# Kernel optimization log

Hardware: AMD Instinct MI355X
Metric: run time of the kernel (lower is better)

The kernel has to match this reference:

```python
import jax, jax.numpy as jnp
import numpy as np

B, N, F, H, OUT = 64, 512, 128, 256, 6


def setup_inputs() -> dict:
    key = jax.random.key(0)
    ks = jax.random.split(key, 20)
    s = 0.02
    inp = {
        "x": jax.random.normal(ks[0], (B * N, F), dtype=jnp.float32),
        "edge_index": jax.random.randint(ks[1], (2, 16), 0, B * N),
        "edge_weight": jax.random.uniform(ks[2], (16,), dtype=jnp.float32),
        "batch": jnp.repeat(jnp.arange(B, dtype=jnp.int64), N),
        "sigma": jax.random.uniform(ks[3], (1,), dtype=jnp.float32),
        "Wg": s * jax.random.normal(ks[4], (F, F)), "bg": jnp.zeros((F,)),
        "Wrel0": s * jax.random.normal(ks[5], (F, H)), "Wroot0": s * jax.random.normal(ks[6], (F, H)), "brel0": jnp.zeros((H,)),
        "Wrel1": s * jax.random.normal(ks[7], (H, H)), "Wroot1": s * jax.random.normal(ks[8], (H, H)), "brel1": jnp.zeros((H,)),
        "Wrel2": s * jax.random.normal(ks[9], (H, H)), "Wroot2": s * jax.random.normal(ks[10], (H, H)), "brel2": jnp.zeros((H,)),
        "W1": s * jax.random.normal(ks[11], (H, H)), "b1": jnp.zeros((H,)),
        "Wout": s * jax.random.normal(ks[12], (H, OUT)), "bout": jnp.zeros((OUT,)),
    }
    return inp


def _forward(x, sigma, Wg, bg, Wrel0, Wroot0, brel0, Wrel1, Wroot1, brel1,
             Wrel2, Wroot2, brel2, W1, b1, Wout, bout):
    # gdmLinear
    h = x @ Wg + bg                      # [B*N, F]
    hw = h.reshape(B, N, -1)             # to_dense_batch (equal-size windows)
    # pairwise squared distances per window -> Gaussian kernel
    sq = jnp.sum(hw * hw, axis=-1)       # [B, N]
    dist = jnp.maximum(sq[:, :, None] + sq[:, None, :]
                       - 2.0 * jnp.einsum('bnf,bmf->bnm', hw, hw), 0.0)
    A = jnp.exp(-dist / (2.0 * sigma[0] ** 2))   # [B, N, N], all > 0
    A = A * (1.0 - jnp.eye(N, dtype=A.dtype))    # nonzero extraction drops self-loops

    def conv(h, Wrel, Wroot, brel):
        # GraphConv: out_i = W_rel @ sum_j A[j,i] * h_j + b_rel + W_root @ h_i
        agg = jnp.einsum('bji,bjf->bif', A, h)
        return agg @ Wrel + brel + h @ Wroot

    h = hw
    h = jax.nn.relu(conv(h, Wrel0, Wroot0, brel0))
    h = jax.nn.relu(conv(h, Wrel1, Wroot1, brel1))
    h = conv(h, Wrel2, Wroot2, brel2)
    g = jnp.mean(h, axis=1)              # global_mean_pool (equal-size graphs)
    g = jax.nn.relu(g @ W1 + b1)
    return g @ Wout + bout               # [B, OUT]


def reference(x, edge_index, edge_weight, batch, sigma, Wg, bg,
              Wrel0, Wroot0, brel0, Wrel1, Wroot1, brel1,
              Wrel2, Wroot2, brel2, W1, b1, Wout, bout):
    # edge_index / edge_weight / batch inputs are recomputed internally by GdmGNN
    return _forward(x, sigma, Wg, bg, Wrel0, Wroot0, brel0, Wrel1, Wroot1, brel1,
                    Wrel2, Wroot2, brel2, W1, b1, Wout, bout)
```

## Files before the change

### kernel.cpp

```cpp
#include <hip/hip_runtime.h>
#include <math.h>

#define Bsz 64
#define Nn 512
#define Ff 128
#define Hh 256
#define OUTD 6
#define MTOT (Bsz * Nn)

typedef __bf16 bf16x8 __attribute__((ext_vector_type(8)));
typedef float f32x4 __attribute__((ext_vector_type(4)));
typedef int int4v __attribute__((ext_vector_type(4)));
typedef unsigned short ushort4v __attribute__((ext_vector_type(4)));

__device__ __forceinline__ unsigned short f2bf(float f) {
    unsigned u = __float_as_uint(f);
    u += 0x7FFFu + ((u >> 16) & 1u);
    return (unsigned short)(u >> 16);
}
__device__ __forceinline__ float bf2f(unsigned short s) {
    return __uint_as_float(((unsigned)s) << 16);
}

#define SWZ(r) (((r) ^ ((r) >> 2)) & 3)

__device__ __forceinline__ void async_ld16(const unsigned short* g, unsigned short* l) {
    __builtin_amdgcn_global_load_lds(
        (const __attribute__((address_space(1))) void*)g,
        (__attribute__((address_space(3))) void*)l,
        16, 0, 0);
}

#define LDH 40
#define TSZ (128 * 32)
#define ATS (256 * 32)
#define AGP 136
#define AGP1 264

__global__ __launch_bounds__(512) void fused_l0(
    const unsigned short* __restrict__ h0T,
    const unsigned short* __restrict__ Arows,
    const unsigned short* __restrict__ h0b,
    const unsigned short* __restrict__ WrelT0,
    const unsigned short* __restrict__ WrootT0,
    const float* __restrict__ brel0,
    unsigned short* __restrict__ h1b,
    unsigned short* __restrict__ h1T)
{
    int id = blockIdx.x;
    int b = id & 63;
    int nt = id >> 6;
    int n0g = nt * 128;
    long nodeBase = (long)b * Nn + n0g;

    const unsigned short* HT = h0T + (long)b * Ff * Nn;
    const unsigned short* AR = Arows + (long)b * Nn * Nn;

    __shared__ unsigned short SA[2 * ATS];
    __shared__ unsigned short SB[2 * TSZ];
    __shared__ unsigned short aggL[128 * AGP];

    int tid = threadIdx.x;
    int lane = tid & 63;
    int wave = tid >> 6;
    int quad = lane >> 4, l16 = lane & 15;
    int sr = lane >> 2, sc = lane & 3;

    {
        int wm = (wave >> 1) * 32, wn = (wave & 1) * 64;
        f32x4 acc[2][4] = {};
        auto issue = [&](int g) {
            int kk = g << 5;
            unsigned short* Ad = SA + (g & 1) * ATS;
            unsigned short* Bd = SB + (g & 1) * TSZ;
            int r = wave * 16 + sr;
            int c = sc ^ SWZ(r);
            async_ld16(HT + (long)r * Nn + kk + c * 8, Ad + (wave * 16) * 32);
            async_ld16(AR + (long)(n0g + r) * Nn + kk + c * 8, Bd + (wave * 16) * 32);
        };
        issue(0);
        for (int g = 0; g < (Nn >> 5); ++g) {
            __syncthreads();
            if (g + 1 < (Nn >> 5)) issue(g + 1);
            const unsigned short* Ab = SA + (g & 1) * ATS;
            const unsigned short* Bb = SB + (g & 1) * TSZ;
            bf16x8 af[2], bfr[4];
            #pragma unroll
            for (int i = 0; i < 2; ++i) {
                int r = wm + i * 16 + l16;
                af[i] = *(const bf16x8*)&Ab[r * 32 + (quad ^ SWZ(r)) * 8];
            }
            #pragma unroll
            for (int j = 0; j < 4; ++j) {
                int r = wn + j * 16 + l16;
                bfr[j] = *(const bf16x8*)&Bb[r * 32 + (quad ^ SWZ(r)) * 8];
            }
            #pragma unroll
            for (int i = 0; i < 2; ++i)
                #pragma unroll
                for (int j = 0; j < 4; ++j)
                    acc[i][j] = __builtin_amdgcn_mfma_f32_16x16x32_bf16(
                        af[i], bfr[j], acc[i][j], 0, 0, 0);
        }
        #pragma unroll
        for (int i = 0; i < 2; ++i) {
            int f = wm + i * 16 + quad * 4;
            #pragma unroll
            for (int j = 0; j < 4; ++j) {
                int nl = wn + j * 16 + l16;
                f32x4 v = acc[i][j];
                ushort4v p;
                p[0] = f2bf(v[0]); p[1] = f2bf(v[1]);
                p[2] = f2bf(v[2]); p[3] = f2bf(v[3]);
                *(ushort4v*)&aggL[nl * AGP + f] = p;
            }
        }
    }
    __syncthreads();

    {
        int wm = (wave >> 1) * 64, wn = (wave & 1) * 64;
        f32x4 acc[4][4] = {};
        auto issue2 = [&](int g) {
            const unsigned short* Wp = (g < 4) ? WrelT0 : WrootT0;
            int kk = (g & 3) << 5;
            unsigned short* Ad = SA + (g & 1) * ATS;
            int r = wave * 16 + sr;
            int c = sc ^ SWZ(r);
            async_ld16(Wp + (long)r * Ff + kk + c * 8, Ad + (wave * 16) * 32);
            int r2 = 128 + r;
            int c2 = sc ^ SWZ(r2);
            async_ld16(Wp + (long)r2 * Ff + kk + c2 * 8, Ad + (128 + wave * 16) * 32);
            if (g >= 4) {
                unsigned short* Bd = SB + (g & 1) * TSZ;
                async_ld16(h0b + (nodeBase + r) * Ff + kk + c * 8,
                           Bd + (wave * 16) * 32);
            }
        };
        issue2(0);
        for (int g = 0; g < 8; ++g) {
            __syncthreads();
            if (g + 1 < 8) issue2(g + 1);
            const unsigned short* Ab = SA + (g & 1) * ATS;
            bf16x8 af[4], bfr[4];
            #pragma unroll
            for (int i = 0; i < 4; ++i) {
                int r = wm + i * 16 + l16;
                af[i] = *(const bf16x8*)&Ab[r * 32 + (quad ^ SWZ(r)) * 8];
            }
            if (g < 4) {
                #pragma unroll
                for (int j = 0; j < 4; ++j) {
                    int nl = wn + j * 16 + l16;
                    bfr[j] = *(const bf16x8*)&aggL[nl * AGP + (g << 5) + quad * 8];
                }
            } else {
                const unsigned short* Bb = SB + (g & 1) * TSZ;
                #pragma unroll
                for (int j = 0; j < 4; ++j) {
                    int r = wn + j * 16 + l16;
                    bfr[j] = *(const bf16x8*)&Bb[r * 32 + (quad ^ SWZ(r)) * 8];
                }
            }
            #pragma unroll
            for (int i = 0; i < 4; ++i)
                #pragma unroll
                for (int j = 0; j < 4; ++j)
                    acc[i][j] = __builtin_amdgcn_mfma_f32_16x16x32_bf16(
                        af[i], bfr[j], acc[i][j], 0, 0, 0);
        }
        #pragma unroll
        for (int i = 0; i < 4; ++i) {
            int of = wm + i * 16 + quad * 4;
            float b0 = brel0[of + 0], b1 = brel0[of + 1];
            float b2 = brel0[of + 2], b3 = brel0[of + 3];
            #pragma unroll
            for (int j = 0; j < 4; ++j) {
                int nl = wn + j * 16 + l16;
                f32x4 v = acc[i][j];
                float o0 = fmaxf(v[0] + b0, 0.f), o1 = fmaxf(v[1] + b1, 0.f);
                float o2 = fmaxf(v[2] + b2, 0.f), o3 = fmaxf(v[3] + b3, 0.f);
                ushort4v p;
                p[0] = f2bf(o0); p[1] = f2bf(o1); p[2] = f2bf(o2); p[3] = f2bf(o3);
                *(ushort4v*)&h1b[(nodeBase + nl) * Hh + of] = p;
                long base = ((long)b * Hh) * 512 + n0g + nl;
                h1T[base + (long)(of + 0) * 512] = p[0];
                h1T[base + (long)(of + 1) * 512] = p[1];
                h1T[base + (long)(of + 2) * 512] = p[2];
                h1T[base + (long)(of + 3) * 512] = p[3];
            }
        }
    }
}

__global__ __launch_bounds__(512) void fused_l1(
    const unsigned short* __restrict__ h1T,
    const unsigned short* __restrict__ Arows,
    const unsigned short* __restrict__ h1b,
    const unsigned short* __restrict__ WrelT1,
    const unsigned short* __restrict__ WrootT1,
    const float* __restrict__ brel1,
    const float* __restrict__ w,
    float* __restrict__ vpart, float* __restrict__ mpart)
{
    constexpr int BTS = 128 * 32;

    int id = blockIdx.x;
    int b = id & 63;
    int nt = id >> 6;
    int n0g = nt * 128;
    long nodeBase = (long)b * Nn + n0g;

    const unsigned short* HT = h1T + (long)b * Hh * Nn;
    const unsigned short* AR = Arows + (long)b * Nn * Nn;

    __shared__ unsigned short SA[2 * ATS];
    __shared__ unsigned short SB[2 * BTS];
    __shared__ unsigned short aggL[128 * AGP1];

    int tid = threadIdx.x;
    int lane = tid & 63;
    int wave = tid >> 6;
    int quad = lane >> 4, l16 = lane & 15;
    int wm = (wave >> 1) * 64;
    int wn = (wave & 1) * 64;
    int sr = lane >> 2, sc = lane & 3;

    {
        f32x4 acc[4][4] = {};
        auto issue = [&](int g) {
            int kk = g << 5;
            unsigned short* Ad = SA + (g & 1) * ATS;
            int r = wave * 16 + sr;
            int c = sc ^ SWZ(r);
            async_ld16(HT + (long)r * Nn + kk + c * 8, Ad + (wave * 16) * 32);
            int r2 = 128 + r;
            int c2 = sc ^ SWZ(r2);
            async_ld16(HT + (long)r2 * Nn + kk + c2 * 8, Ad + (128 + wave * 16) * 32);
            unsigned short* Bd = SB + (g & 1) * BTS;
            async_ld16(AR + (long)(n0g + r) * Nn + kk + c * 8, Bd + (wave * 16) * 32);
        };
        issue(0);
        for (int g = 0; g < 16; ++g) {
            __syncthreads();
            if (g + 1 < 16) issue(g + 1);
            const unsigned short* Ab = SA + (g & 1) * ATS;
            const unsigned short* Bb = SB + (g & 1) * BTS;
            bf16x8 af[4], bfr[4];
            #pragma unroll
            for (int i = 0; i < 4; ++i) {
                int r = wm + i * 16 + l16;
                af[i] = *(const bf16x8*)&Ab[r * 32 + (quad ^ SWZ(r)) * 8];
            }
            #pragma unroll
            for (int j = 0; j < 4; ++j) {
                int r = wn + j * 16 + l16;
                bfr[j] = *(const bf16x8*)&Bb[r * 32 + (quad ^ SWZ(r)) * 8];
            }
            #pragma unroll
            for (int i = 0; i < 4; ++i)
                #pragma unroll
                for (int j = 0; j < 4; ++j)
                    acc[i][j] = __builtin_amdgcn_mfma_f32_16x16x32_bf16(
                        af[i], bfr[j], acc[i][j], 0, 0, 0);
        }
        #pragma unroll
        for (int i = 0; i < 4; ++i) {
            int f = wm + i * 16 + quad * 4;
            #pragma unroll
            for (int j = 0; j < 4; ++j) {
                int nl = wn + j * 16 + l16;
                f32x4 v = acc[i][j];
                ushort4v p;
                p[0] = f2bf(v[0]); p[1] = f2bf(v[1]);
                p[2] = f2bf(v[2]); p[3] = f2bf(v[3]);
                *(ushort4v*)&aggL[nl * AGP1 + f] = p;
            }
        }
    }
    __syncthreads();

    f32x4 acc[4][4] = {};
    auto issue2 = [&](int g) {
        const unsigned short* Wp = (g < 8) ? WrelT1 : WrootT1;
        int kk = (g & 7) << 5;
        unsigned short* Ad = SA + (g & 1) * ATS;
        int r = wave * 16 + sr;
        int c = sc ^ SWZ(r);
        async_ld16(Wp + (long)r * Hh + kk + c * 8, Ad + (wave * 16) * 32);
        int r2 = 128 + r;
        int c2 = sc ^ SWZ(r2);
        async_ld16(Wp + (long)r2 * Hh + kk + c2 * 8, Ad + (128 + wave * 16) * 32);
        if (g >= 8) {
            unsigned short* Bd = SB + (g & 1) * BTS;
            async_ld16(h1b + (nodeBase + r) * Hh + kk + c * 8, Bd + (wave * 16) * 32);
        }
    };
    issue2(0);
    for (int g = 0; g < 16; ++g) {
        __syncthreads();
        if (g + 1 < 16) issue2(g + 1);
        const unsigned short* Ab = SA + (g & 1) * ATS;
        bf16x8 af[4], bfr[4];
        #pragma unroll
        for (int i = 0; i < 4; ++i) {
            int r = wm + i * 16 + l16;
            af[i] = *(const bf16x8*)&Ab[r * 32 + (quad ^ SWZ(r)) * 8];
        }
        if (g < 8) {
            #pragma unroll
            for (int j = 0; j < 4; ++j) {
                int nl = wn + j * 16 + l16;
                bfr[j] = *(const bf16x8*)&aggL[nl * AGP1 + (g << 5) + quad * 8];
            }
        } else {
            const unsigned short* Bb = SB + (g & 1) * BTS;
            #pragma unroll
            for (int j = 0; j < 4; ++j) {
                int r = wn + j * 16 + l16;
                bfr[j] = *(const bf16x8*)&Bb[r * 32 + (quad ^ SWZ(r)) * 8];
            }
        }
        #pragma unroll
        for (int i = 0; i < 4; ++i)
            #pragma unroll
            for (int j = 0; j < 4; ++j)
                acc[i][j] = __builtin_amdgcn_mfma_f32_16x16x32_bf16(
                    af[i], bfr[j], acc[i][j], 0, 0, 0);
    }

    #pragma unroll
    for (int i = 0; i < 4; ++i) {
        int lf = wm + i * 16 + quad * 4;
        float b0 = brel1[lf + 0], b1 = brel1[lf + 1];
        float b2 = brel1[lf + 2], b3 = brel1[lf + 3];
        float vp0 = 0.f, vp1 = 0.f, vp2 = 0.f, vp3 = 0.f;
        float mp0 = 0.f, mp1 = 0.f, mp2 = 0.f, mp3 = 0.f;
        #pragma unroll
        for (int j = 0; j < 4; ++j) {
            long node = nodeBase + wn + j * 16 + l16;
            f32x4 v = acc[i][j];
            float o0 = fmaxf(v[0] + b0, 0.f), o1 = fmaxf(v[1] + b1, 0.f);
            float o2 = fmaxf(v[2] + b2, 0.f), o3 = fmaxf(v[3] + b3, 0.f);
            float h0v = bf2f(f2bf(o0)), h1v = bf2f(f2bf(o1));
            float h2v = bf2f(f2bf(o2)), h3v = bf2f(f2bf(o3));
            float wv = w[node];
            vp0 += wv * h0v; vp1 += wv * h1v; vp2 += wv * h2v; vp3 += wv * h3v;
            mp0 += h0v; mp1 += h1v; mp2 += h2v; mp3 += h3v;
        }
        #pragma unroll
        for (int m = 1; m < 16; m <<= 1) {
            vp0 += __shfl_xor(vp0, m); vp1 += __shfl_xor(vp1, m);
            vp2 += __shfl_xor(vp2, m); vp3 += __shfl_xor(vp3, m);
            mp0 += __shfl_xor(mp0, m); mp1 += __shfl_xor(mp1, m);
            mp2 += __shfl_xor(mp2, m); mp3 += __shfl_xor(mp3, m);
        }
        if (l16 == 0) {
            long o = ((long)(b * 8 + nt * 2 + (wave & 1))) * Hh + lf;
            float4 vv = {vp0, vp1, vp2, vp3};
            float4 mm = {mp0, mp1, mp2, mp3};
            *(float4*)&vpart[o] = vv;
            *(float4*)&mpart[o] = mm;
        }
    }
}

__global__ __launch_bounds__(256) void prep_h0(
    const float* __restrict__ x, const float* __restrict__ Wg,
    const float* __restrict__ bg,
    const float* __restrict__ Wrel0, const float* __restrict__ Wroot0,
    const float* __restrict__ Wrel1, const float* __restrict__ Wroot1,
    unsigned short* __restrict__ T0, unsigned short* __restrict__ T1,
    unsigned short* __restrict__ T2, unsigned short* __restrict__ T3,
    float* __restrict__ w,
    unsigned short* __restrict__ h0b, unsigned short* __restrict__ h0T,
    float* __restrict__ sqv)
{
    if (blockIdx.x < 896) {
        int idx = blockIdx.x * 256 + threadIdx.x;
        if (idx >= 196608) { w[idx - 196608] = 0.f; return; }
        const float* src; unsigned short* dst; int kin; int e;
        if      (idx <  32768) { src = Wrel0;  dst = T0; kin = 128; e = idx; }
        else if (idx <  65536) { src = Wroot0; dst = T1; kin = 128; e = idx - 32768; }
        else if (idx < 131072) { src = Wrel1;  dst = T2; kin = 256; e = idx - 65536; }
        else                   { src = Wroot1; dst = T3; kin = 256; e = idx - 131072; }
        int o = (kin == 128) ? (e >> 7) : (e >> 8);
        int i = e & (kin - 1);
        dst[e] = f2bf(src[(long)i * 256 + o]);
        return;
    }

    __shared__ unsigned short As[128 * LDH];
    __shared__ unsigned short Bs[128 * LDH];
    __shared__ float rsq[128];

    int tid = threadIdx.x;
    int lane = tid & 63;
    int wave = tid >> 6;
    int quad = lane >> 4, l16 = lane & 15;
    int wm = (wave >> 1) * 64, wn = (wave & 1) * 64;
    int m0 = (blockIdx.x - 896) * 128;

    f32x4 acc[4][4] = {};

    for (int k0 = 0; k0 < Ff; k0 += 32) {
        __syncthreads();
        #pragma unroll
        for (int l = 0; l < 2; ++l) {
            int idx = tid + l * 256;
            int r = idx >> 2, ch = idx & 3;
            const float* px = x + (long)(m0 + r) * Ff + k0 + ch * 8;
            float4 xa = *(const float4*)px;
            float4 xb = *(const float4*)(px + 4);
            ushort4v pa, pb;
            pa[0] = f2bf(xa.x); pa[1] = f2bf(xa.y); pa[2] = f2bf(xa.z); pa[3] = f2bf(xa.w);
            pb[0] = f2bf(xb.x); pb[1] = f2bf(xb.y); pb[2] = f2bf(xb.z); pb[3] = f2bf(xb.w);
            *(ushort4v*)&As[r * LDH + ch * 8] = pa;
            *(ushort4v*)&As[r * LDH + ch * 8 + 4] = pb;
            int kk = k0 + ch * 8;
            ushort4v qa, qb;
            #pragma unroll
            for (int u = 0; u < 4; ++u) qa[u] = f2bf(Wg[(long)(kk + u) * 128 + r]);
            #pragma unroll
            for (int u = 0; u < 4; ++u) qb[u] = f2bf(Wg[(long)(kk + 4 + u) * 128 + r]);
            *(ushort4v*)&Bs[r * LDH + ch * 8] = qa;
            *(ushort4v*)&Bs[r * LDH + ch * 8 + 4] = qb;
        }
        __syncthreads();
        bf16x8 af[4], bfr[4];
        #pragma unroll
        for (int i = 0; i < 4; ++i)
            af[i] = *(const bf16x8*)&As[(wm + i * 16 + l16) * LDH + quad * 8];
        #pragma unroll
        for (int j = 0; j < 4; ++j)
            bfr[j] = *(const bf16x8*)&Bs[(wn + j * 16 + l16) * LDH + quad * 8];
        #pragma unroll
        for (int i = 0; i < 4; ++i)
            #pragma unroll
            for (int j = 0; j < 4; ++j)
                acc[i][j] = __builtin_amdgcn_mfma_f32_16x16x32_bf16(
                    af[i], bfr[j], acc[i][j], 0, 0, 0);
    }

    if (tid < 128) rsq[tid] = 0.f;
    __syncthreads();

    #pragma unroll
    for (int i = 0; i < 4; ++i) {
        int lrow = wm + i * 16 + quad * 4;
        int mb = m0 + lrow;
        float rp0 = 0.f, rp1 = 0.f, rp2 = 0.f, rp3 = 0.f;
        #pragma unroll
        for (int j = 0; j < 4; ++j) {
            int n = wn + j * 16 + l16;
            f32x4 v = acc[i][j];
            float bv = bg[n];
            unsigned short s0 = f2bf(v[0] + bv), s1 = f2bf(v[1] + bv);
            unsigned short s2 = f2bf(v[2] + bv), s3 = f2bf(v[3] + bv);
            h0b[(long)(mb + 0) * Ff + n] = s0;
            h0b[(long)(mb + 1) * Ff + n] = s1;
            h0b[(long)(mb + 2) * Ff + n] = s2;
            h0b[(long)(mb + 3) * Ff + n] = s3;
            ushort4v p; p[0] = s0; p[1] = s1; p[2] = s2; p[3] = s3;
            long ti = ((long)(mb >> 9) * Ff + n) * 512 + (mb & 511);
            *(ushort4v*)&h0T[ti] = p;
            float f0 = bf2f(s0), f1 = bf2f(s1), f2 = bf2f(s2), f3 = bf2f(s3);
            rp0 += f0 * f0; rp1 += f1 * f1; rp2 += f2 * f2; rp3 += f3 * f3;
        }
        #pragma unroll
        for (int m = 1; m < 16; m <<= 1) {
            rp0 += __shfl_xor(rp0, m);
            rp1 += __shfl_xor(rp1, m);
            rp2 += __shfl_xor(rp2, m);
            rp3 += __shfl_xor(rp3, m);
        }
        if (l16 == 0) {
            atomicAdd(&rsq[lrow + 0], rp0);
            atomicAdd(&rsq[lrow + 1], rp1);
            atomicAdd(&rsq[lrow + 2], rp2);
            atomicAdd(&rsq[lrow + 3], rp3);
        }
    }
    __syncthreads();
    if (tid < 128) sqv[m0 + tid] = rsq[tid];
}

__global__ __launch_bounds__(512) void gram_A_mfma(
    const unsigned short* __restrict__ h0b, const float* __restrict__ sqv,
    const float* __restrict__ sigma, unsigned short* __restrict__ Aout,
    float* __restrict__ w)
{
    int id = blockIdx.x;
    int b = id & 63;
    int t = id >> 6;
    int i0 = (t & 3) * 128, j0 = (t >> 2) * 128;

    const unsigned short* H = h0b + (long)b * Nn * Ff;
    const float* SQ = sqv + (long)b * Nn;
    unsigned short* Ab = Aout + (long)b * Nn * Nn;

    __shared__ unsigned short Is[2 * TSZ];
    __shared__ unsigned short Js[2 * TSZ];
    __shared__ float rsum[128];

    int tid = threadIdx.x;
    int lane = tid & 63;
    int wave = tid >> 6;
    int quad = lane >> 4, l16 = lane & 15;
    int wm = (wave >> 1) * 32, wn = (wave & 1) * 64;

    int sr = lane >> 2, sc = lane & 3;

    f32x4 acc[2][4] = {};

    auto issue = [&](int g) {
        int kk = g << 5;
        unsigned short* Id = Is + (g & 1) * TSZ;
        unsigned short* Jd = Js + (g & 1) * TSZ;
        int r = wave * 16 + sr;
        int c = sc ^ SWZ(r);
        async_ld16(H + (long)(i0 + r) * Ff + kk + c * 8, Id + (wave * 16) * 32);
        async_ld16(H + (long)(j0 + r) * Ff + kk + c * 8, Jd + (wave * 16) * 32);
    };

    issue(0);
    for (int g = 0; g < (Ff >> 5); ++g) {
        __syncthreads();
        if (g + 1 < (Ff >> 5)) issue(g + 1);
        const unsigned short* Ib = Is + (g & 1) * TSZ;
        const unsigned short* Jb = Js + (g & 1) * TSZ;
        bf16x8 af[2], bfr[4];
        #pragma unroll
        for (int i = 0; i < 2; ++i) {
            int r = wm + i * 16 + l16;
            af[i] = *(const bf16x8*)&Ib[r * 32 + (quad ^ SWZ(r)) * 8];
        }
        #pragma unroll
        for (int j = 0; j < 4; ++j) {
            int r = wn + j * 16 + l16;
            bfr[j] = *(const bf16x8*)&Jb[r * 32 + (quad ^ SWZ(r)) * 8];
        }
        #pragma unroll
        for (int i = 0; i < 2; ++i)
            #pragma unroll
            for (int j = 0; j < 4; ++j)
                acc[i][j] = __builtin_amdgcn_mfma_f32_16x16x32_bf16(
                    af[i], bfr[j], acc[i][j], 0, 0, 0);
    }

    if (tid < 128) rsum[tid] = 0.f;
    __syncthreads();

    float s = sigma[0];
    float inv2s2 = 1.0f / (2.0f * s * s);
    #pragma unroll
    for (int i = 0; i < 2; ++i) {
        int lrow = wm + i * 16 + quad * 4;
        int rb = i0 + lrow;
        float rs0 = 0.f, rs1 = 0.f, rs2 = 0.f, rs3 = 0.f;
        #pragma unroll
        for (int j = 0; j < 4; ++j) {
            int c = j0 + wn + j * 16 + l16;
            float sqc = SQ[c];
            f32x4 v = acc[i][j];
            ushort4v pk;
            float av[4];
            #pragma unroll
            for (int r4 = 0; r4 < 4; ++r4) {
                int r = rb + r4;
                float d = fmaxf(SQ[r] + sqc - 2.0f * v[r4], 0.0f);
                unsigned short a = (r == c) ? (unsigned short)0
                                            : f2bf(__expf(-d * inv2s2));
                pk[r4] = a;
                av[r4] = bf2f(a);
            }
            *(ushort4v*)&Ab[(long)c * Nn + rb] = pk;
            rs0 += av[0]; rs1 += av[1]; rs2 += av[2]; rs3 += av[3];
        }
        #pragma unroll
        for (int m = 1; m < 16; m <<= 1) {
            rs0 += __shfl_xor(rs0, m);
            rs1 += __shfl_xor(rs1, m);
            rs2 += __shfl_xor(rs2, m);
            rs3 += __shfl_xor(rs3, m);
        }
        if (l16 == 0) {
            atomicAdd(&rsum[lrow + 0], rs0);
            atomicAdd(&rsum[lrow + 1], rs1);
            atomicAdd(&rsum[lrow + 2], rs2);
            atomicAdd(&rsum[lrow + 3], rs3);
        }
    }
    __syncthreads();
    if (tid < 128) atomicAdd(&w[(long)b * Nn + i0 + tid], rsum[tid]);
}

__global__ __launch_bounds__(256) void head_kernel(
    const float* __restrict__ vpart, const float* __restrict__ mpart,
    const float* __restrict__ Wrel2, const float* __restrict__ Wroot2,
    const float* __restrict__ brel2,
    const float* __restrict__ W1, const float* __restrict__ b1,
    const float* __restrict__ Wout, const float* __restrict__ bout,
    float* __restrict__ out)
{
    int b = blockIdx.x;
    int j = threadIdx.x;
    __shared__ float vs[Hh], ms[Hh], gs[Hh], g2[Hh];
    float vp = 0.f, mp = 0.f;
    #pragma unroll
    for (int p = 0; p < 8; ++p) {
        long o = ((long)(b * 8 + p)) * Hh + j;
        vp += vpart[o];
        mp += mpart[o];
    }
    vs[j] = vp * (1.0f / (float)Nn);
    ms[j] = mp * (1.0f / (float)Nn);
    __syncthreads();
    float s = brel2[j];
    for (int c = 0; c < Hh; ++c)
        s += vs[c] * Wrel2[c * Hh + j] + ms[c] * Wroot2[c * Hh + j];
    gs[j] = s;
    __syncthreads();
    float t = b1[j];
    for (int k = 0; k < Hh; ++k) t += gs[k] * W1[k * Hh + j];
    g2[j] = fmaxf(t, 0.f);
    __syncthreads();
    if (j < OUTD) {
        float s2 = bout[j];
        for (int k = 0; k < Hh; ++k) s2 += g2[k] * Wout[k * OUTD + j];
        out[b * OUTD + j] = s2;
    }
}

extern "C" void kernel_launch(void* const* d_in, const int* in_sizes, int n_in,
                              void* d_out, int out_size, void* d_ws, size_t ws_size,
                              hipStream_t stream) {
    const float* x      = (const float*)d_in[0];
    const float* sigma  = (const float*)d_in[4];
    const float* Wg     = (const float*)d_in[5];
    const float* bg     = (const float*)d_in[6];
    const float* Wrel0  = (const float*)d_in[7];
    const float* Wroot0 = (const float*)d_in[8];
    const float* brel0  = (const float*)d_in[9];
    const float* Wrel1  = (const float*)d_in[10];
    const float* Wroot1 = (const float*)d_in[11];
    const float* brel1  = (const float*)d_in[12];
    const float* Wrel2  = (const float*)d_in[13];
    const float* Wroot2 = (const float*)d_in[14];
    const float* brel2  = (const float*)d_in[15];
    const float* W1     = (const float*)d_in[16];
    const float* b1     = (const float*)d_in[17];
    const float* Wout   = (const float*)d_in[18];
    const float* bout   = (const float*)d_in[19];
    float* out = (float*)d_out;

    char* ws = (char*)d_ws;
    unsigned short* h0b  = (unsigned short*)(ws + 16777216);
    unsigned short* h0T  = (unsigned short*)(ws + 25165824);
    float*          sq   = (float*)(ws + 33554432);
    unsigned short* Aadj = (unsigned short*)(ws + 33685504);
    unsigned short* h1b  = (unsigned short*)(ws + 84017152);
    unsigned short* h1T  = (unsigned short*)(ws + 100794368);
    unsigned short* WrelT0  = (unsigned short*)(ws + 167903232);
    unsigned short* WrootT0 = (unsigned short*)(ws + 167968768);
    unsigned short* WrelT1  = (unsigned short*)(ws + 168034304);
    unsigned short* WrootT1 = (unsigned short*)(ws + 168165376);
    float*          w     = (float*)(ws + 168558592);
    float*          vpart = (float*)(ws + 168689664);
    float*          mpart = (float*)(ws + 169213952);

    prep_h0<<<1152, 256, 0, stream>>>(x, Wg, bg, Wrel0, Wroot0, Wrel1, Wroot1,
                                      WrelT0, WrootT0, WrelT1, WrootT1,
                                      w, h0b, h0T, sq);

    gram_A_mfma<<<dim3(16 * Bsz, 1, 1), 512, 0, stream>>>(h0b, sq, sigma, Aadj, w);

    fused_l0<<<dim3(4 * Bsz, 1, 1), 512, 0, stream>>>(
        h0T, Aadj, h0b, WrelT0, WrootT0, brel0, h1b, h1T);

    fused_l1<<<dim3(4 * Bsz, 1, 1), 512, 0, stream>>>(
        h1T, Aadj, h1b, WrelT1, WrootT1, brel1, w, vpart, mpart);

    head_kernel<<<Bsz, 256, 0, stream>>>(vpart, mpart, Wrel2, Wroot2, brel2,
                                         W1, b1, Wout, bout, out);
}
```

Before: 211.5 us.

## Merge all stages into one cooperative persistent kernel with grid syncs

Replaces the five separate launches (prep, gram/adjacency, layer0, layer1, head) with a single cooperative kernel of 256 blocks that separates the stages with grid.sync. The aim is to remove launch gaps and tail effects between the small kernels. In exchange, the gram stage now runs with 256 blocks looping over 4 tiles each instead of 1024 blocks. The prep stage uses only 256 blocks as well. Each grid barrier adds its own cost.

```diff
diff --git a/kernel.cpp b/kernel.cpp
--- a/kernel.cpp
+++ b/kernel.cpp
@@ -1,16 +1,17 @@
 #include <hip/hip_runtime.h>
+#include <hip/hip_cooperative_groups.h>
 #include <math.h>
+
+namespace cg = cooperative_groups;
 
 #define Bsz 64
 #define Nn 512
 #define Ff 128
 #define Hh 256
 #define OUTD 6
-#define MTOT (Bsz * Nn)
 
 typedef __bf16 bf16x8 __attribute__((ext_vector_type(8)));
 typedef float f32x4 __attribute__((ext_vector_type(4)));
-typedef int int4v __attribute__((ext_vector_type(4)));
 typedef unsigned short ushort4v __attribute__((ext_vector_type(4)));
 
 __device__ __forceinline__ unsigned short f2bf(float f) {
@@ -32,69 +33,105 @@
 }
 
 #define LDH 40
-#define TSZ (128 * 32)
-#define ATS (256 * 32)
 #define AGP 136
 #define AGP1 264
 
-__global__ __launch_bounds__(512) void fused_l0(
-    const unsigned short* __restrict__ h0T,
-    const unsigned short* __restrict__ Arows,
-    const unsigned short* __restrict__ h0b,
-    const unsigned short* __restrict__ WrelT0,
-    const unsigned short* __restrict__ WrootT0,
+__global__ __launch_bounds__(512) void mega(
+    const float* __restrict__ x, const float* __restrict__ sigma,
+    const float* __restrict__ Wg, const float* __restrict__ bg,
+    const float* __restrict__ Wrel0, const float* __restrict__ Wroot0,
     const float* __restrict__ brel0,
-    unsigned short* __restrict__ h1b,
-    unsigned short* __restrict__ h1T)
+    const float* __restrict__ Wrel1, const float* __restrict__ Wroot1,
+    const float* __restrict__ brel1,
+    const float* __restrict__ Wrel2, const float* __restrict__ Wroot2,
+    const float* __restrict__ brel2,
+    const float* __restrict__ W1, const float* __restrict__ b1,
+    const float* __restrict__ Wout, const float* __restrict__ bout,
+    float* __restrict__ out, char* __restrict__ ws)
 {
-    int id = blockIdx.x;
-    int b = id & 63;
-    int nt = id >> 6;
-    int n0g = nt * 128;
-    long nodeBase = (long)b * Nn + n0g;
-
-    const unsigned short* HT = h0T + (long)b * Ff * Nn;
-    const unsigned short* AR = Arows + (long)b * Nn * Nn;
-
-    __shared__ unsigned short SA[2 * ATS];
-    __shared__ unsigned short SB[2 * TSZ];
-    __shared__ unsigned short aggL[128 * AGP];
-
+    unsigned short* h0b  = (unsigned short*)(ws + 16777216);
+    unsigned short* h0T  = (unsigned short*)(ws + 25165824);
+    float*          sq   = (float*)(ws + 33554432);
+    unsigned short* Aadj = (unsigned short*)(ws + 33685504);
+    unsigned short* h1b  = (unsigned short*)(ws + 84017152);
+    unsigned short* h1T  = (unsigned short*)(ws + 100794368);
+    unsigned short* T0   = (unsigned short*)(ws + 167903232);
+    unsigned short* T1   = (unsigned short*)(ws + 167968768);
+    unsigned short* T2   = (unsigned short*)(ws + 168034304);
+    unsigned short* T3   = (unsigned short*)(ws + 168165376);
+    float*          w     = (float*)(ws + 168558592);
+    float*          vpart = (float*)(ws + 168689664);
+    float*          mpart = (float*)(ws + 169213952);
+
+    cg::grid_group grid = cg::this_grid();
+
+    __shared__ __align__(16) unsigned char SMEM[116736];
+
+    int blk = blockIdx.x;
     int tid = threadIdx.x;
     int lane = tid & 63;
     int wave = tid >> 6;
     int quad = lane >> 4, l16 = lane & 15;
     int sr = lane >> 2, sc = lane & 3;
+    int b = blk & 63;
 
     {
+        int gid = blk * 512 + tid;
+        #pragma unroll
+        for (int it = 0; it < 2; ++it) {
+            int idx = gid + it * 131072;
+            if (idx < 196608) {
+                const float* src; unsigned short* dst; int kin; int e;
+                if      (idx <  32768) { src = Wrel0;  dst = T0; kin = 128; e = idx; }
+                else if (idx <  65536) { src = Wroot0; dst = T1; kin = 128; e = idx - 32768; }
+                else if (idx < 131072) { src = Wrel1;  dst = T2; kin = 256; e = idx - 65536; }
+                else                   { src = Wroot1; dst = T3; kin = 256; e = idx - 131072; }
+                int o = (kin == 128) ? (e >> 7) : (e >> 8);
+                int i = e & (kin - 1);
+                dst[e] = f2bf(src[(long)i * 256 + o]);
+            } else if (idx < 229376) {
+                w[idx - 196608] = 0.f;
+            }
+        }
+    }
+
+    {
+        unsigned short* As = (unsigned short*)SMEM;
+        unsigned short* Bs = As + 128 * LDH;
+        float* rsq = (float*)(SMEM + 20480);
+        int m0 = blk * 128;
         int wm = (wave >> 1) * 32, wn = (wave & 1) * 64;
         f32x4 acc[2][4] = {};
-        auto issue = [&](int g) {
-            int kk = g << 5;
-            unsigned short* Ad = SA + (g & 1) * ATS;
-            unsigned short* Bd = SB + (g & 1) * TSZ;
-            int r = wave * 16 + sr;
-            int c = sc ^ SWZ(r);
-            async_ld16(HT + (long)r * Nn + kk + c * 8, Ad + (wave * 16) * 32);
-            async_ld16(AR + (long)(n0g + r) * Nn + kk + c * 8, Bd + (wave * 16) * 32);
-        };
-        issue(0);
-        for (int g = 0; g < (Nn >> 5); ++g) {
+
+        for (int k0 = 0; k0 < Ff; k0 += 32) {
             __syncthreads();
-            if (g + 1 < (Nn >> 5)) issue(g + 1);
-            const unsigned short* Ab = SA + (g & 1) * ATS;
-            const unsigned short* Bb = SB + (g & 1) * TSZ;
+            {
+                int r = tid >> 2, ch = tid & 3;
+                const float* px = x + (long)(m0 + r) * Ff + k0 + ch * 8;
+                float4 xa = *(const float4*)px;
+                float4 xb = *(const float4*)(px + 4);
+                ushort4v pa, pb;
+                pa[0] = f2bf(xa.x); pa[1] = f2bf(xa.y); pa[2] = f2bf(xa.z); pa[3] = f2bf(xa.w);
+                pb[0] = f2bf(xb.x); pb[1] = f2bf(xb.y); pb[2] = f2bf(xb.z); pb[3] = f2bf(xb.w);
+                *(ushort4v*)&As[r * LDH + ch * 8] = pa;
+                *(ushort4v*)&As[r * LDH + ch * 8 + 4] = pb;
+                int kk = k0 + ch * 8;
+                ushort4v qa, qb;
+                #pragma unroll
+                for (int u = 0; u < 4; ++u) qa[u] = f2bf(Wg[(long)(kk + u) * 128 + r]);
+                #pragma unroll
+                for (int u = 0; u < 4; ++u) qb[u] = f2bf(Wg[(long)(kk + 4 + u) * 128 + r]);
+                *(ushort4v*)&Bs[r * LDH + ch * 8] = qa;
+                *(ushort4v*)&Bs[r * LDH + ch * 8 + 4] = qb;
+            }
+            __syncthreads();
             bf16x8 af[2], bfr[4];
             #pragma unroll
-            for (int i = 0; i < 2; ++i) {
-                int r = wm + i * 16 + l16;
-                af[i] = *(const bf16x8*)&Ab[r * 32 + (quad ^ SWZ(r)) * 8];
-            }
-            #pragma unroll
-            for (int j = 0; j < 4; ++j) {
-                int r = wn + j * 16 + l16;
-                bfr[j] = *(const bf16x8*)&Bb[r * 32 + (quad ^ SWZ(r)) * 8];
-            }
+            for (int i = 0; i < 2; ++i)
+                af[i] = *(const bf16x8*)&As[(wm + i * 16 + l16) * LDH + quad * 8];
+            #pragma unroll
+            for (int j = 0; j < 4; ++j)
+                bfr[j] = *(const bf16x8*)&Bs[(wn + j * 16 + l16) * LDH + quad * 8];
             #pragma unroll
             for (int i = 0; i < 2; ++i)
                 #pragma unroll
@@ -102,60 +139,394 @@
                     acc[i][j] = __builtin_amdgcn_mfma_f32_16x16x32_bf16(
                         af[i], bfr[j], acc[i][j], 0, 0, 0);
         }
+
+        if (tid < 128) rsq[tid] = 0.f;
+        __syncthreads();
+
         #pragma unroll
         for (int i = 0; i < 2; ++i) {
-            int f = wm + i * 16 + quad * 4;
+            int lrow = wm + i * 16 + quad * 4;
+            int mb = m0 + lrow;
+            float rp0 = 0.f, rp1 = 0.f, rp2 = 0.f, rp3 = 0.f;
             #pragma unroll
             for (int j = 0; j < 4; ++j) {
-                int nl = wn + j * 16 + l16;
+                int n = wn + j * 16 + l16;
                 f32x4 v = acc[i][j];
-                ushort4v p;
-                p[0] = f2bf(v[0]); p[1] = f2bf(v[1]);
-                p[2] = f2bf(v[2]); p[3] = f2bf(v[3]);
-                *(ushort4v*)&aggL[nl * AGP + f] = p;
-            }
-        }
+                float bv = bg[n];
+                unsigned short s0 = f2bf(v[0] + bv), s1 = f2bf(v[1] + bv);
+                unsigned short s2 = f2bf(v[2] + bv), s3 = f2bf(v[3] + bv);
+                h0b[(long)(mb + 0) * Ff + n] = s0;
+                h0b[(long)(mb + 1) * Ff + n] = s1;
+                h0b[(long)(mb + 2) * Ff + n] = s2;
+                h0b[(long)(mb + 3) * Ff + n] = s3;
+                ushort4v p; p[0] = s0; p[1] = s1; p[2] = s2; p[3] = s3;
+                long ti = ((long)(mb >> 9) * Ff + n) * 512 + (mb & 511);
+                *(ushort4v*)&h0T[ti] = p;
+                float f0 = bf2f(s0), f1 = bf2f(s1), f2 = bf2f(s2), f3 = bf2f(s3);
+                rp0 += f0 * f0; rp1 += f1 * f1; rp2 += f2 * f2; rp3 += f3 * f3;
+            }
+            #pragma unroll
+            for (int m = 1; m < 16; m <<= 1) {
+                rp0 += __shfl_xor(rp0, m);
+                rp1 += __shfl_xor(rp1, m);
+                rp2 += __shfl_xor(rp2, m);
+                rp3 += __shfl_xor(rp3, m);
+            }
+            if (l16 == 0) {
+                atomicAdd(&rsq[lrow + 0], rp0);
+                atomicAdd(&rsq[lrow + 1], rp1);
+                atomicAdd(&rsq[lrow + 2], rp2);
+                atomicAdd(&rsq[lrow + 3], rp3);
+            }
+        }
+        __syncthreads();
+        if (tid < 128) sq[m0 + tid] = rsq[tid];
     }
-    __syncthreads();
+    __threadfence();
+    grid.sync();
+    __threadfence();
 
     {
-        int wm = (wave >> 1) * 64, wn = (wave & 1) * 64;
+        unsigned short* Is = (unsigned short*)SMEM;
+        unsigned short* Js = Is + 8192;
+        float* rsum = (float*)(SMEM + 32768);
+        const unsigned short* H = h0b + (long)b * Nn * Ff;
+        const float* SQ = sq + (long)b * Nn;
+        unsigned short* Ab = Aadj + (long)b * Nn * Nn;
+        float s = sigma[0];
+        float inv2s2 = 1.0f / (2.0f * s * s);
+        int wm = (wave >> 1) * 32, wn = (wave & 1) * 64;
+
+        for (int t2 = 0; t2 < 4; ++t2) {
+            int t = (blk >> 6) + t2 * 4;
+            int i0 = (t & 3) * 128, j0 = (t >> 2) * 128;
+            __syncthreads();
+
+            f32x4 acc[2][4] = {};
+            auto issue = [&](int g) {
+                int kk = g << 5;
+                unsigned short* Id = Is + (g & 1) * 4096;
+                unsigned short* Jd = Js + (g & 1) * 4096;
+                int r = wave * 16 + sr;
+                int c = sc ^ SWZ(r);
+                async_ld16(H + (long)(i0 + r) * Ff + kk + c * 8, Id + (wave * 16) * 32);
+                async_ld16(H + (long)(j0 + r) * Ff + kk + c * 8, Jd + (wave * 16) * 32);
+            };
+            issue(0);
+            for (int g = 0; g < 4; ++g) {
+                __syncthreads();
+                if (g + 1 < 4) issue(g + 1);
+                const unsigned short* Ib = Is + (g & 1) * 4096;
+                const unsigned short* Jb = Js + (g & 1) * 4096;
+                bf16x8 af[2], bfr[4];
+                #pragma unroll
+                for (int i = 0; i < 2; ++i) {
+                    int r = wm + i * 16 + l16;
+                    af[i] = *(const bf16x8*)&Ib[r * 32 + (quad ^ SWZ(r)) * 8];
+                }
+                #pragma unroll
+                for (int j = 0; j < 4; ++j) {
+                    int r = wn + j * 16 + l16;
+                    bfr[j] = *(const bf16x8*)&Jb[r * 32 + (quad ^ SWZ(r)) * 8];
+                }
+                #pragma unroll
+                for (int i = 0; i < 2; ++i)
+                    #pragma unroll
+                    for (int j = 0; j < 4; ++j)
+                        acc[i][j] = __builtin_amdgcn_mfma_f32_16x16x32_bf16(
+                            af[i], bfr[j], acc[i][j], 0, 0, 0);
+            }
+
+            if (tid < 128) rsum[tid] = 0.f;
+            __syncthreads();
+
+            #pragma unroll
+            for (int i = 0; i < 2; ++i) {
+                int lrow = wm + i * 16 + quad * 4;
+                int rb = i0 + lrow;
+                float rs0 = 0.f, rs1 = 0.f, rs2 = 0.f, rs3 = 0.f;
+                #pragma unroll
+                for (int j = 0; j < 4; ++j) {
+                    int c = j0 + wn + j * 16 + l16;
+                    float sqc = SQ[c];
+                    f32x4 v = acc[i][j];
+                    ushort4v pk;
+                    float av[4];
+                    #pragma unroll
+                    for (int r4 = 0; r4 < 4; ++r4) {
+                        int r = rb + r4;
+                        float d = fmaxf(SQ[r] + sqc - 2.0f * v[r4], 0.0f);
+                        unsigned short a = (r == c) ? (unsigned short)0
+                                                    : f2bf(__expf(-d * inv2s2));
+                        pk[r4] = a;
+                        av[r4] = bf2f(a);
+                    }
+                    *(ushort4v*)&Ab[(long)c * Nn + rb] = pk;
+                    rs0 += av[0]; rs1 += av[1]; rs2 += av[2]; rs3 += av[3];
+                }
+                #pragma unroll
+                for (int m = 1; m < 16; m <<= 1) {
+                    rs0 += __shfl_xor(rs0, m);
+                    rs1 += __shfl_xor(rs1, m);
+                    rs2 += __shfl_xor(rs2, m);
+                    rs3 += __shfl_xor(rs3, m);
+                }
+                if (l16 == 0) {
+                    atomicAdd(&rsum[lrow + 0], rs0);
+                    atomicAdd(&rsum[lrow + 1], rs1);
+                    atomicAdd(&rsum[lrow + 2], rs2);
+                    atomicAdd(&rsum[lrow + 3], rs3);
+                }
+            }
+            __syncthreads();
+            if (tid < 128) atomicAdd(&w[(long)b * Nn + i0 + tid], rsum[tid]);
+        }
+    }
+    __threadfence();
+    grid.sync();
+    __threadfence();
+
+    {
+        unsigned short* SA = (unsigned short*)SMEM;
+        unsigned short* SB = SA + 16384;
+        unsigned short* aggL = SB + 8192;
+        int nt = blk >> 6;
+        int n0g = nt * 128;
+        long nodeBase = (long)b * Nn + n0g;
+        const unsigned short* HT = h0T + (long)b * Ff * Nn;
+        const unsigned short* AR = Aadj + (long)b * Nn * Nn;
+
+        {
+            int wm = (wave >> 1) * 32, wn = (wave & 1) * 64;
+            f32x4 acc[2][4] = {};
+            auto issue = [&](int g) {
+                int kk = g << 5;
+                unsigned short* Ad = SA + (g & 1) * 8192;
+                unsigned short* Bd = SB + (g & 1) * 4096;
+                int r = wave * 16 + sr;
+                int c = sc ^ SWZ(r);
+                async_ld16(HT + (long)r * Nn + kk + c * 8, Ad + (wave * 16) * 32);
+                async_ld16(AR + (long)(n0g + r) * Nn + kk + c * 8, Bd + (wave * 16) * 32);
+            };
+            issue(0);
+            for (int g = 0; g < 16; ++g) {
+                __syncthreads();
+                if (g + 1 < 16) issue(g + 1);
+                const unsigned short* Ab = SA + (g & 1) * 8192;
+                const unsigned short* Bb = SB + (g & 1) * 4096;
+                bf16x8 af[2], bfr[4];
+                #pragma unroll
+                for (int i = 0; i < 2; ++i) {
+                    int r = wm + i * 16 + l16;
+                    af[i] = *(const bf16x8*)&Ab[r * 32 + (quad ^ SWZ(r)) * 8];
+                }
+                #pragma unroll
+                for (int j = 0; j < 4; ++j) {
+                    int r = wn + j * 16 + l16;
+                    bfr[j] = *(const bf16x8*)&Bb[r * 32 + (quad ^ SWZ(r)) * 8];
+                }
+                #pragma unroll
+                for (int i = 0; i < 2; ++i)
+                    #pragma unroll
+                    for (int j = 0; j < 4; ++j)
+                        acc[i][j] = __builtin_amdgcn_mfma_f32_16x16x32_bf16(
+                            af[i], bfr[j], acc[i][j], 0, 0, 0);
+            }
+            #pragma unroll
+            for (int i = 0; i < 2; ++i) {
+                int f = wm + i * 16 + quad * 4;
+                #pragma unroll
+                for (int j = 0; j < 4; ++j) {
+                    int nl = wn + j * 16 + l16;
+                    f32x4 v = acc[i][j];
+                    ushort4v p;
+                    p[0] = f2bf(v[0]); p[1] = f2bf(v[1]);
+                    p[2] = f2bf(v[2]); p[3] = f2bf(v[3]);
+                    *(ushort4v*)&aggL[nl * AGP + f] = p;
+                }
+            }
+        }
+        __syncthreads();
+
+        {
+            int wm = (wave >> 1) * 64, wn = (wave & 1) * 64;
+            f32x4 acc[4][4] = {};
+            auto issue2 = [&](int g) {
+                const unsigned short* Wp = (g < 4) ? T0 : T1;
+                int kk = (g & 3) << 5;
+                unsigned short* Ad = SA + (g & 1) * 8192;
+                int r = wave * 16 + sr;
+                int c = sc ^ SWZ(r);
+                async_ld16(Wp + (long)r * Ff + kk + c * 8, Ad + (wave * 16) * 32);
+                int r2 = 128 + r;
+                int c2 = sc ^ SWZ(r2);
+                async_ld16(Wp + (long)r2 * Ff + kk + c2 * 8, Ad + (128 + wave * 16) * 32);
+                if (g >= 4) {
+                    unsigned short* Bd = SB + (g & 1) * 4096;
+                    async_ld16(h0b + (nodeBase + r) * Ff + kk + c * 8,
+                               Bd + (wave * 16) * 32);
+                }
+            };
+            issue2(0);
+            for (int g = 0; g < 8; ++g) {
+                __syncthreads();
+                if (g + 1 < 8) issue2(g + 1);
+                const unsigned short* Ab = SA + (g & 1) * 8192;
+                bf16x8 af[4], bfr[4];
+                #pragma unroll
+                for (int i = 0; i < 4; ++i) {
+                    int r = wm + i * 16 + l16;
+                    af[i] = *(const bf16x8*)&Ab[r * 32 + (quad ^ SWZ(r)) * 8];
+                }
+                if (g < 4) {
+                    #pragma unroll
+                    for (int j = 0; j < 4; ++j) {
+                        int nl = wn + j * 16 + l16;
+                        bfr[j] = *(const bf16x8*)&aggL[nl * AGP + (g << 5) + quad * 8];
+                    }
+                } else {
+                    const unsigned short* Bb = SB + (g & 1) * 4096;
+                    #pragma unroll
+                    for (int j = 0; j < 4; ++j) {
+                        int r = wn + j * 16 + l16;
+                        bfr[j] = *(const bf16x8*)&Bb[r * 32 + (quad ^ SWZ(r)) * 8];
+                    }
+                }
+                #pragma unroll
+                for (int i = 0; i < 4; ++i)
+                    #pragma unroll
+                    for (int j = 0; j < 4; ++j)
+                        acc[i][j] = __builtin_amdgcn_mfma_f32_16x16x32_bf16(
+                            af[i], bfr[j], acc[i][j], 0, 0, 0);
+            }
+            #pragma unroll
+            for (int i = 0; i < 4; ++i) {
+                int of = wm + i * 16 + quad * 4;
+                float b0 = brel0[of + 0], b1 = brel0[of + 1];
+                float b2 = brel0[of + 2], b3 = brel0[of + 3];
+                #pragma unroll
+                for (int j = 0; j < 4; ++j) {
+                    int nl = wn + j * 16 + l16;
+                    f32x4 v = acc[i][j];
+                    float o0 = fmaxf(v[0] + b0, 0.f), o1 = fmaxf(v[1] + b1, 0.f);
+                    float o2 = fmaxf(v[2] + b2, 0.f), o3 = fmaxf(v[3] + b3, 0.f);
+                    ushort4v p;
+                    p[0] = f2bf(o0); p[1] = f2bf(o1); p[2] = f2bf(o2); p[3] = f2bf(o3);
+                    *(ushort4v*)&h1b[(nodeBase + nl) * Hh + of] = p;
+                    long base = ((long)b * Hh) * 512 + n0g + nl;
+                    h1T[base + (long)(of + 0) * 512] = p[0];
+                    h1T[base + (long)(of + 1) * 512] = p[1];
+                    h1T[base + (long)(of + 2) * 512] = p[2];
+                    h1T[base + (long)(of + 3) * 512] = p[3];
+                }
+            }
+        }
+    }
+    __threadfence();
+    grid.sync();
+    __threadfence();
+
+    {
+        unsigned short* SA = (unsigned short*)SMEM;
+        unsigned short* SB = SA + 16384;
+        unsigned short* aggL = SB + 8192;
+        int nt = blk >> 6;
+        int n0g = nt * 128;
+        long nodeBase = (long)b * Nn + n0g;
+        const unsigned short* HT = h1T + (long)b * Hh * Nn;
+        const unsigned short* AR = Aadj + (long)b * Nn * Nn;
+        int wm = (wave >> 1) * 64;
+        int wn = (wave & 1) * 64;
+
+        {
+            f32x4 acc[4][4] = {};
+            auto issue = [&](int g) {
+                int kk = g << 5;
+                unsigned short* Ad = SA + (g & 1) * 8192;
+                int r = wave * 16 + sr;
+                int c = sc ^ SWZ(r);
+                async_ld16(HT + (long)r * Nn + kk + c * 8, Ad + (wave * 16) * 32);
+                int r2 = 128 + r;
+                int c2 = sc ^ SWZ(r2);
+                async_ld16(HT + (long)r2 * Nn + kk + c2 * 8, Ad + (128 + wave * 16) * 32);
+                unsigned short* Bd = SB + (g & 1) * 4096;
+                async_ld16(AR + (long)(n0g + r) * Nn + kk + c * 8, Bd + (wave * 16) * 32);
+            };
+            issue(0);
+            for (int g = 0; g < 16; ++g) {
+                __syncthreads();
+                if (g + 1 < 16) issue(g + 1);
+                const unsigned short* Ab = SA + (g & 1) * 8192;
+                const unsigned short* Bb = SB + (g & 1) * 4096;
+                bf16x8 af[4], bfr[4];
+                #pragma unroll
+                for (int i = 0; i < 4; ++i) {
+                    int r = wm + i * 16 + l16;
+                    af[i] = *(const bf16x8*)&Ab[r * 32 + (quad ^ SWZ(r)) * 8];
+                }
+                #pragma unroll
+                for (int j = 0; j < 4; ++j) {
+                    int r = wn + j * 16 + l16;
+                    bfr[j] = *(const bf16x8*)&Bb[r * 32 + (quad ^ SWZ(r)) * 8];
+                }
+                #pragma unroll
+                for (int i = 0; i < 4; ++i)
+                    #pragma unroll
+                    for (int j = 0; j < 4; ++j)
+                        acc[i][j] = __builtin_amdgcn_mfma_f32_16x16x32_bf16(
+                            af[i], bfr[j], acc[i][j], 0, 0, 0);
+            }
+            #pragma unroll
+            for (int i = 0; i < 4; ++i) {
+                int f = wm + i * 16 + quad * 4;
+                #pragma unroll
+                for (int j = 0; j < 4; ++j) {
+                    int nl = wn + j * 16 + l16;
+                    f32x4 v = acc[i][j];
+                    ushort4v p;
+                    p[0] = f2bf(v[0]); p[1] = f2bf(v[1]);
+                    p[2] = f2bf(v[2]); p[3] = f2bf(v[3]);
+                    *(ushort4v*)&aggL[nl * AGP1 + f] = p;
+                }
+            }
+        }
+        __syncthreads();
+
         f32x4 acc[4][4] = {};
         auto issue2 = [&](int g) {
-            const unsigned short* Wp = (g < 4) ? WrelT0 : WrootT0;
-            int kk = (g & 3) << 5;
-            unsigned short* Ad = SA + (g & 1) * ATS;
+            const unsigned short* Wp = (g < 8) ? T2 : T3;
+            int kk = (g & 7) << 5;
+            unsigned short* Ad = SA + (g & 1) * 8192;
             int r = wave * 16 + sr;
             int c = sc ^ SWZ(r);
-            async_ld16(Wp + (long)r * Ff + kk + c * 8, Ad + (wave * 16) * 32);
+            async_ld16(Wp + (long)r * Hh + kk + c * 8, Ad + (wave * 16) * 32);
             int r2 = 128 + r;
             int c2 = sc ^ SWZ(r2);
-            async_ld16(Wp + (long)r2 * Ff + kk + c2 * 8, Ad + (128 + wave * 16) * 32);
-            if (g >= 4) {
-                unsigned short* Bd = SB + (g & 1) * TSZ;
-                async_ld16(h0b + (nodeBase + r) * Ff + kk + c * 8,
-                           Bd + (wave * 16) * 32);
+            async_ld16(Wp + (long)r2 * Hh + kk + c2 * 8, Ad + (128 + wave * 16) * 32);
+            if (g >= 8) {
+                unsigned short* Bd = SB + (g & 1) * 4096;
+                async_ld16(h1b + (nodeBase + r) * Hh + kk + c * 8, Bd + (wave * 16) * 32);
             }
         };
         issue2(0);
-        for (int g = 0; g < 8; ++g) {
+        for (int g = 0; g < 16; ++g) {
             __syncthreads();
-            if (g + 1 < 8) issue2(g + 1);
-            const unsigned short* Ab = SA + (g & 1) * ATS;
+            if (g + 1 < 16) issue2(g + 1);
+            const unsigned short* Ab = SA + (g & 1) * 8192;
             bf16x8 af[4], bfr[4];
             #pragma unroll
             for (int i = 0; i < 4; ++i) {
                 int r = wm + i * 16 + l16;
                 af[i] = *(const bf16x8*)&Ab[r * 32 + (quad ^ SWZ(r)) * 8];
             }
-            if (g < 4) {
+            if (g < 8) {
                 #pragma unroll
                 for (int j = 0; j < 4; ++j) {
                     int nl = wn + j * 16 + l16;
-                    bfr[j] = *(const bf16x8*)&aggL[nl * AGP + (g << 5) + quad * 8];
+                    bfr[j] = *(const bf16x8*)&aggL[nl * AGP1 + (g << 5) + quad * 8];
                 }
             } else {
-                const unsigned short* Bb = SB + (g & 1) * TSZ;
+                const unsigned short* Bb = SB + (g & 1) * 4096;
                 #pragma unroll
                 for (int j = 0; j < 4; ++j) {
                     int r = wn + j * 16 + l16;
@@ -169,466 +540,83 @@
                     acc[i][j] = __builtin_amdgcn_mfma_f32_16x16x32_bf16(
                         af[i], bfr[j], acc[i][j], 0, 0, 0);
         }
+
         #pragma unroll
         for (int i = 0; i < 4; ++i) {
-            int of = wm + i * 16 + quad * 4;
-            float b0 = brel0[of + 0], b1 = brel0[of + 1];
-            float b2 = brel0[of + 2], b3 = brel0[of + 3];
+            int lf = wm + i * 16 + quad * 4;
+            float b0 = brel1[lf + 0], b1 = brel1[lf + 1];
+            float b2 = brel1[lf + 2], b3 = brel1[lf + 3];
+            float vp0 = 0.f, vp1 = 0.f, vp2 = 0.f, vp3 = 0.f;
+            float mp0 = 0.f, mp1 = 0.f, mp2 = 0.f, mp3 = 0.f;
             #pragma unroll
             for (int j = 0; j < 4; ++j) {
-                int nl = wn + j * 16 + l16;
+                long node = nodeBase + wn + j * 16 + l16;
                 f32x4 v = acc[i][j];
                 float o0 = fmaxf(v[0] + b0, 0.f), o1 = fmaxf(v[1] + b1, 0.f);
                 float o2 = fmaxf(v[2] + b2, 0.f), o3 = fmaxf(v[3] + b3, 0.f);
-                ushort4v p;
-                p[0] = f2bf(o0); p[1] = f2bf(o1); p[2] = f2bf(o2); p[3] = f2bf(o3);
-                *(ushort4v*)&h1b[(nodeBase + nl) * Hh + of] = p;
-                long base = ((long)b * Hh) * 512 + n0g + nl;
-                h1T[base + (long)(of + 0) * 512] = p[0];
-                h1T[base + (long)(of + 1) * 512] = p[1];
-                h1T[base + (long)(of + 2) * 512] = p[2];
-                h1T[base + (long)(of + 3) * 512] = p[3];
+                float h0v = bf2f(f2bf(o0)), h1v = bf2f(f2bf(o1));
+                float h2v = bf2f(f2bf(o2)), h3v = bf2f(f2bf(o3));
+                float wv = w[node];
+                vp0 += wv * h0v; vp1 += wv * h1v; vp2 += wv * h2v; vp3 += wv * h3v;
+                mp0 += h0v; mp1 += h1v; mp2 += h2v; mp3 += h3v;
+            }
+            #pragma unroll
+            for (int m = 1; m < 16; m <<= 1) {
+                vp0 += __shfl_xor(vp0, m); vp1 += __shfl_xor(vp1, m);
+                vp2 += __shfl_xor(vp2, m); vp3 += __shfl_xor(vp3, m);
+                mp0 += __shfl_xor(mp0, m); mp1 += __shfl_xor(mp1, m);
+                mp2 += __shfl_xor(mp2, m); mp3 += __shfl_xor(mp3, m);
+            }
+            if (l16 == 0) {
+                long o = ((long)(b * 8 + nt * 2 + (wave & 1))) * Hh + lf;
+                float4 vv = {vp0, vp1, vp2, vp3};
+                float4 mm = {mp0, mp1, mp2, mp3};
+                *(float4*)&vpart[o] = vv;
+                *(float4*)&mpart[o] = mm;
             }
         }
     }
-}
-
-__global__ __launch_bounds__(512) void fused_l1(
-    const unsigned short* __restrict__ h1T,
-    const unsigned short* __restrict__ Arows,
-    const unsigned short* __restrict__ h1b,
-    const unsigned short* __restrict__ WrelT1,
-    const unsigned short* __restrict__ WrootT1,
-    const float* __restrict__ brel1,
-    const float* __restrict__ w,
-    float* __restrict__ vpart, float* __restrict__ mpart)
-{
-    constexpr int BTS = 128 * 32;
-
-    int id = blockIdx.x;
-    int b = id & 63;
-    int nt = id >> 6;
-    int n0g = nt * 128;
-    long nodeBase = (long)b * Nn + n0g;
-
-    const unsigned short* HT = h1T + (long)b * Hh * Nn;
-    const unsigned short* AR = Arows + (long)b * Nn * Nn;
-
-    __shared__ unsigned short SA[2 * ATS];
-    __shared__ unsigned short SB[2 * BTS];
-    __shared__ unsigned short aggL[128 * AGP1];
-
-    int tid = threadIdx.x;
-    int lane = tid & 63;
-    int wave = tid >> 6;
-    int quad = lane >> 4, l16 = lane & 15;
-    int wm = (wave >> 1) * 64;
-    int wn = (wave & 1) * 64;
-    int sr = lane >> 2, sc = lane & 3;
-
-    {
-        f32x4 acc[4][4] = {};
-        auto issue = [&](int g) {
-            int kk = g << 5;
-            unsigned short* Ad = SA + (g & 1) * ATS;
-            int r = wave * 16 + sr;
-            int c = sc ^ SWZ(r);
-            async_ld16(HT + (long)r * Nn + kk + c * 8, Ad + (wave * 16) * 32);
-            int r2 = 128 + r;
-            int c2 = sc ^ SWZ(r2);
-            async_ld16(HT + (long)r2 * Nn + kk + c2 * 8, Ad + (128 + wave * 16) * 32);
-            unsigned short* Bd = SB + (g & 1) * BTS;
-            async_ld16(AR + (long)(n0g + r) * Nn + kk + c * 8, Bd + (wave * 16) * 32);
-        };
-        issue(0);
-        for (int g = 0; g < 16; ++g) {
-            __syncthreads();
-            if (g + 1 < 16) issue(g + 1);
-            const unsigned short* Ab = SA + (g & 1) * ATS;
-            const unsigned short* Bb = SB + (g & 1) * BTS;
-            bf16x8 af[4], bfr[4];
-            #pragma unroll
-            for (int i = 0; i < 4; ++i) {
-                int r = wm + i * 16 + l16;
-                af[i] = *(const bf16x8*)&Ab[r * 32 + (quad ^ SWZ(r)) * 8];
-            }
-            #pragma unroll
-            for (int j = 0; j < 4; ++j) {
-                int r = wn + j * 16 + l16;
-                bfr[j] = *(const bf16x8*)&Bb[r * 32 + (quad ^ SWZ(r)) * 8];
-            }
-            #pragma unroll
-            for (int i = 0; i < 4; ++i)
-                #pragma unroll
-                for (int j = 0; j < 4; ++j)
-                    acc[i][j] = __builtin_amdgcn_mfma_f32_16x16x32_bf16(
-                        af[i], bfr[j], acc[i][j], 0, 0, 0);
-        }
-        #pragma unroll
-        for (int i = 0; i < 4; ++i) {
-            int f = wm + i * 16 + quad * 4;
-            #pragma unroll
-            for (int j = 0; j < 4; ++j) {
-                int nl = wn + j * 16 + l16;
-                f32x4 v = acc[i][j];
-                ushort4v p;
-                p[0] = f2bf(v[0]); p[1] = f2bf(v[1]);
-                p[2] = f2bf(v[2]); p[3] = f2bf(v[3]);
-                *(ushort4v*)&aggL[nl * AGP1 + f] = p;
-            }
-        }
-    }
-    __syncthreads();
-
-    f32x4 acc[4][4] = {};
-    auto issue2 = [&](int g) {
-        const unsigned short* Wp = (g < 8) ? WrelT1 : WrootT1;
-        int kk = (g & 7) << 5;
-        unsigned short* Ad = SA + (g & 1) * ATS;
-        int r = wave * 16 + sr;
-        int c = sc ^ SWZ(r);
-        async_ld16(Wp + (long)r * Hh + kk + c * 8, Ad + (wave * 16) * 32);
-        int r2 = 128 + r;
-        int c2 = sc ^ SWZ(r2);
-        async_ld16(Wp + (long)r2 * Hh + kk + c2 * 8, Ad + (128 + wave * 16) * 32);
-        if (g >= 8) {
-            unsigned short* Bd = SB + (g & 1) * BTS;
-            async_ld16(h1b + (nodeBase + r) * Hh + kk + c * 8, Bd + (wave * 16) * 32);
-        }
-    };
-    issue2(0);
-    for (int g = 0; g < 16; ++g) {
+    __threadfence();
+    grid.sync();
+    __threadfence();
+
+    if (blk < 64) {
+        float* vs = (float*)SMEM;
+        float* ms = vs + Hh;
+        float* gs = ms + Hh;
+        float* g2 = gs + Hh;
+        int j = tid;
+        bool act = (tid < Hh);
+        if (act) {
+            float vp = 0.f, mp = 0.f;
+            #pragma unroll
+            for (int p = 0; p < 8; ++p) {
+                long o = ((long)(blk * 8 + p)) * Hh + j;
+                vp += vpart[o];
+                mp += mpart[o];
+            }
+            vs[j] = vp * (1.0f / (float)Nn);
+            ms[j] = mp * (1.0f / (float)Nn);
+        }
         __syncthreads();
-        if (g + 1 < 16) issue2(g + 1);
-        const unsigned short* Ab = SA + (g & 1) * ATS;
-        bf16x8 af[4], bfr[4];
-        #pragma unroll
-        for (int i = 0; i < 4; ++i) {
-            int r = wm + i * 16 + l16;
-            af[i] = *(const bf16x8*)&Ab[r * 32 + (quad ^ SWZ(r)) * 8];
-        }
-        if (g < 8) {
-            #pragma unroll
-            for (int j = 0; j < 4; ++j) {
-                int nl = wn + j * 16 + l16;
-                bfr[j] = *(const bf16x8*)&aggL[nl * AGP1 + (g << 5) + quad * 8];
-            }
-        } else {
-            const unsigned short* Bb = SB + (g & 1) * BTS;
-            #pragma unroll
-            for (int j = 0; j < 4; ++j) {
-                int r = wn + j * 16 + l16;
-                bfr[j] = *(const bf16x8*)&Bb[r * 32 + (quad ^ SWZ(r)) * 8];
-            }
-        }
-        #pragma unroll
-        for (int i = 0; i < 4; ++i)
-            #pragma unroll
-            for (int j = 0; j < 4; ++j)
-                acc[i][j] = __builtin_amdgcn_mfma_f32_16x16x32_bf16(
-                    af[i], bfr[j], acc[i][j], 0, 0, 0);
-    }
-
-    #pragma unroll
-    for (int i = 0; i < 4; ++i) {
-        int lf = wm + i * 16 + quad * 4;
-        float b0 = brel1[lf + 0], b1 = brel1[lf + 1];
-        float b2 = brel1[lf + 2], b3 = brel1[lf + 3];
-        float vp0 = 0.f, vp1 = 0.f, vp2 = 0.f, vp3 = 0.f;
-        float mp0 = 0.f, mp1 = 0.f, mp2 = 0.f, mp3 = 0.f;
-        #pragma unroll
-        for (int j = 0; j < 4; ++j) {
-            long node = nodeBase + wn + j * 16 + l16;
-            f32x4 v = acc[i][j];
-            float o0 = fmaxf(v[0] + b0, 0.f), o1 = fmaxf(v[1] + b1, 0.f);
-            float o2 = fmaxf(v[2] + b2, 0.f), o3 = fmaxf(v[3] + b3, 0.f);
-            float h0v = bf2f(f2bf(o0)), h1v = bf2f(f2bf(o1));
-            float h2v = bf2f(f2bf(o2)), h3v = bf2f(f2bf(o3));
-            float wv = w[node];
-            vp0 += wv * h0v; vp1 += wv * h1v; vp2 += wv * h2v; vp3 += wv * h3v;
-            mp0 += h0v; mp1 += h1v; mp2 += h2v; mp3 += h3v;
-        }
-        #pragma unroll
-        for (int m = 1; m < 16; m <<= 1) {
-            vp0 += __shfl_xor(vp0, m); vp1 += __shfl_xor(vp1, m);
-            vp2 += __shfl_xor(vp2, m); vp3 += __shfl_xor(vp3, m);
-            mp0 += __shfl_xor(mp0, m); mp1 += __shfl_xor(mp1, m);
-            mp2 += __shfl_xor(mp2, m); mp3 += __shfl_xor(mp3, m);
-        }
-        if (l16 == 0) {
-            long o = ((long)(b * 8 + nt * 2 + (wave & 1))) * Hh + lf;
-            float4 vv = {vp0, vp1, vp2, vp3};
-            float4 mm = {mp0, mp1, mp2, mp3};
-            *(float4*)&vpart[o] = vv;
-            *(float4*)&mpart[o] = mm;
-        }
-    }
-}
-
-__global__ __launch_bounds__(256) void prep_h0(
-    const float* __restrict__ x, const float* __restrict__ Wg,
-    const float* __restrict__ bg,
-    const float* __restrict__ Wrel0, const float* __restrict__ Wroot0,
-    const float* __restrict__ Wrel1, const float* __restrict__ Wroot1,
-    unsigned short* __restrict__ T0, unsigned short* __restrict__ T1,
-    unsigned short* __restrict__ T2, unsigned short* __restrict__ T3,
-    float* __restrict__ w,
-    unsigned short* __restrict__ h0b, unsigned short* __restrict__ h0T,
-    float* __restrict__ sqv)
-{
-    if (blockIdx.x < 896) {
-        int idx = blockIdx.x * 256 + threadIdx.x;
-        if (idx >= 196608) { w[idx - 196608] = 0.f; return; }
-        const float* src; unsigned short* dst; int kin; int e;
-        if      (idx <  32768) { src = Wrel0;  dst = T0; kin = 128; e = idx; }
-        else if (idx <  65536) { src = Wroot0; dst = T1; kin = 128; e = idx - 32768; }
-        else if (idx < 131072) { src = Wrel1;  dst = T2; kin = 256; e = idx - 65536; }
-        else                   { src = Wroot1; dst = T3; kin = 256; e = idx - 131072; }
-        int o = (kin == 128) ? (e >> 7) : (e >> 8);
-        int i = e & (kin - 1);
-        dst[e] = f2bf(src[(long)i * 256 + o]);
-        return;
-    }
-
-    __shared__ unsigned short As[128 * LDH];
-    __shared__ unsigned short Bs[128 * LDH];
-    __shared__ float rsq[128];
-
-    int tid = threadIdx.x;
-    int lane = tid & 63;
-    int wave = tid >> 6;
-    int quad = lane >> 4, l16 = lane & 15;
-    int wm = (wave >> 1) * 64, wn = (wave & 1) * 64;
-    int m0 = (blockIdx.x - 896) * 128;
-
-    f32x4 acc[4][4] = {};
-
-    for (int k0 = 0; k0 < Ff; k0 += 32) {
+        if (act) {
+            float s = brel2[j];
+            for (int c = 0; c < Hh; ++c)
+                s += vs[c] * Wrel2[c * Hh + j] + ms[c] * Wroot2[c * Hh + j];
+            gs[j] = s;
+        }
         __syncthreads();
-        #pragma unroll
-        for (int l = 0; l < 2; ++l) {
-            int idx = tid + l * 256;
-            int r = idx >> 2, ch = idx & 3;
-            const float* px = x + (long)(m0 + r) * Ff + k0 + ch * 8;
-            float4 xa = *(const float4*)px;
-            float4 xb = *(const float4*)(px + 4);
-            ushort4v pa, pb;
-            pa[0] = f2bf(xa.x); pa[1] = f2bf(xa.y); pa[2] = f2bf(xa.z); pa[3] = f2bf(xa.w);
-            pb[0] = f2bf(xb.x); pb[1] = f2bf(xb.y); pb[2] = f2bf(xb.z); pb[3] = f2bf(xb.w);
-            *(ushort4v*)&As[r * LDH + ch * 8] = pa;
-            *(ushort4v*)&As[r * LDH + ch * 8 + 4] = pb;
-            int kk = k0 + ch * 8;
-            ushort4v qa, qb;
-            #pragma unroll
-            for (int u = 0; u < 4; ++u) qa[u] = f2bf(Wg[(long)(kk + u) * 128 + r]);
-            #pragma unroll
-            for (int u = 0; u < 4; ++u) qb[u] = f2bf(Wg[(long)(kk + 4 + u) * 128 + r]);
-            *(ushort4v*)&Bs[r * LDH + ch * 8] = qa;
-            *(ushort4v*)&Bs[r * LDH + ch * 8 + 4] = qb;
+        if (act) {
+            float t = b1[j];
+            for (int k = 0; k < Hh; ++k) t += gs[k] * W1[k * Hh + j];
+            g2[j] = fmaxf(t, 0.f);
         }
         __syncthreads();
-        bf16x8 af[4], bfr[4];
-        #pragma unroll
-        for (int i = 0; i < 4; ++i)
-            af[i] = *(const bf16x8*)&As[(wm + i * 16 + l16) * LDH + quad * 8];
-        #pragma unroll
-        for (int j = 0; j < 4; ++j)
-            bfr[j] = *(const bf16x8*)&Bs[(wn + j * 16 + l16) * LDH + quad * 8];
-        #pragma unroll
-        for (int i = 0; i < 4; ++i)
-            #pragma unroll
-            for (int j = 0; j < 4; ++j)
-                acc[i][j] = __builtin_amdgcn_mfma_f32_16x16x32_bf16(
-                    af[i], bfr[j], acc[i][j], 0, 0, 0);
-    }
-
-    if (tid < 128) rsq[tid] = 0.f;
-    __syncthreads();
-
-    #pragma unroll
-    for (int i = 0; i < 4; ++i) {
-        int lrow = wm + i * 16 + quad * 4;
-        int mb = m0 + lrow;
-        float rp0 = 0.f, rp1 = 0.f, rp2 = 0.f, rp3 = 0.f;
-        #pragma unroll
-        for (int j = 0; j < 4; ++j) {
-            int n = wn + j * 16 + l16;
-            f32x4 v = acc[i][j];
-            float bv = bg[n];
-            unsigned short s0 = f2bf(v[0] + bv), s1 = f2bf(v[1] + bv);
-            unsigned short s2 = f2bf(v[2] + bv), s3 = f2bf(v[3] + bv);
-            h0b[(long)(mb + 0) * Ff + n] = s0;
-            h0b[(long)(mb + 1) * Ff + n] = s1;
-            h0b[(long)(mb + 2) * Ff + n] = s2;
-            h0b[(long)(mb + 3) * Ff + n] = s3;
-            ushort4v p; p[0] = s0; p[1] = s1; p[2] = s2; p[3] = s3;
-            long ti = ((long)(mb >> 9) * Ff + n) * 512 + (mb & 511);
-            *(ushort4v*)&h0T[ti] = p;
-            float f0 = bf2f(s0), f1 = bf2f(s1), f2 = bf2f(s2), f3 = bf2f(s3);
-            rp0 += f0 * f0; rp1 += f1 * f1; rp2 += f2 * f2; rp3 += f3 * f3;
-        }
-        #pragma unroll
-        for (int m = 1; m < 16; m <<= 1) {
-            rp0 += __shfl_xor(rp0, m);
-            rp1 += __shfl_xor(rp1, m);
-            rp2 += __shfl_xor(rp2, m);
-            rp3 += __shfl_xor(rp3, m);
-        }
-        if (l16 == 0) {
-            atomicAdd(&rsq[lrow + 0], rp0);
-            atomicAdd(&rsq[lrow + 1], rp1);
-            atomicAdd(&rsq[lrow + 2], rp2);
-            atomicAdd(&rsq[lrow + 3], rp3);
-        }
-    }
-    __syncthreads();
-    if (tid < 128) sqv[m0 + tid] = rsq[tid];
-}
-
-__global__ __launch_bounds__(512) void gram_A_mfma(
-    const unsigned short* __restrict__ h0b, const float* __restrict__ sqv,
-    const float* __restrict__ sigma, unsigned short* __restrict__ Aout,
-    float* __restrict__ w)
-{
-    int id = blockIdx.x;
-    int b = id & 63;
-    int t = id >> 6;
-    int i0 = (t & 3) * 128, j0 = (t >> 2) * 128;
-
-    const unsigned short* H = h0b + (long)b * Nn * Ff;
-    const float* SQ = sqv + (long)b * Nn;
-    unsigned short* Ab = Aout + (long)b * Nn * Nn;
-
-    __shared__ unsigned short Is[2 * TSZ];
-    __shared__ unsigned short Js[2 * TSZ];
-    __shared__ float rsum[128];
-
-    int tid = threadIdx.x;
-    int lane = tid & 63;
-    int wave = tid >> 6;
-    int quad = lane >> 4, l16 = lane & 15;
-    int wm = (wave >> 1) * 32, wn = (wave & 1) * 64;
-
-    int sr = lane >> 2, sc = lane & 3;
-
-    f32x4 acc[2][4] = {};
-
-    auto issue = [&](int g) {
-        int kk = g << 5;
-        unsigned short* Id = Is + (g & 1) * TSZ;
-        unsigned short* Jd = Js + (g & 1) * TSZ;
-        int r = wave * 16 + sr;
-        int c = sc ^ SWZ(r);
-        async_ld16(H + (long)(i0 + r) * Ff + kk + c * 8, Id + (wave * 16) * 32);
-        async_ld16(H + (long)(j0 + r) * Ff + kk + c * 8, Jd + (wave * 16) * 32);
-    };
-
-    issue(0);
-    for (int g = 0; g < (Ff >> 5); ++g) {
-        __syncthreads();
-        if (g + 1 < (Ff >> 5)) issue(g + 1);
-        const unsigned short* Ib = Is + (g & 1) * TSZ;
-        const unsigned short* Jb = Js + (g & 1) * TSZ;
-        bf16x8 af[2], bfr[4];
-        #pragma unroll
-        for (int i = 0; i < 2; ++i) {
-            int r = wm + i * 16 + l16;
-            af[i] = *(const bf16x8*)&Ib[r * 32 + (quad ^ SWZ(r)) * 8];
-        }
-        #pragma unroll
-        for (int j = 0; j < 4; ++j) {
-            int r = wn + j * 16 + l16;
-            bfr[j] = *(const bf16x8*)&Jb[r * 32 + (quad ^ SWZ(r)) * 8];
-        }
-        #pragma unroll
-        for (int i = 0; i < 2; ++i)
-            #pragma unroll
-            for (int j = 0; j < 4; ++j)
-                acc[i][j] = __builtin_amdgcn_mfma_f32_16x16x32_bf16(
-                    af[i], bfr[j], acc[i][j], 0, 0, 0);
-    }
-
-    if (tid < 128) rsum[tid] = 0.f;
-    __syncthreads();
-
-    float s = sigma[0];
-    float inv2s2 = 1.0f / (2.0f * s * s);
-    #pragma unroll
-    for (int i = 0; i < 2; ++i) {
-        int lrow = wm + i * 16 + quad * 4;
-        int rb = i0 + lrow;
-        float rs0 = 0.f, rs1 = 0.f, rs2 = 0.f, rs3 = 0.f;
-        #pragma unroll
-        for (int j = 0; j < 4; ++j) {
-            int c = j0 + wn + j * 16 + l16;
-            float sqc = SQ[c];
-            f32x4 v = acc[i][j];
-            ushort4v pk;
-            float av[4];
-            #pragma unroll
-            for (int r4 = 0; r4 < 4; ++r4) {
-                int r = rb + r4;
-                float d = fmaxf(SQ[r] + sqc - 2.0f * v[r4], 0.0f);
-                unsigned short a = (r == c) ? (unsigned short)0
-                                            : f2bf(__expf(-d * inv2s2));
-                pk[r4] = a;
-                av[r4] = bf2f(a);
-            }
-            *(ushort4v*)&Ab[(long)c * Nn + rb] = pk;
-            rs0 += av[0]; rs1 += av[1]; rs2 += av[2]; rs3 += av[3];
-        }
-        #pragma unroll
-        for (int m = 1; m < 16; m <<= 1) {
-            rs0 += __shfl_xor(rs0, m);
-            rs1 += __shfl_xor(rs1, m);
-            rs2 += __shfl_xor(rs2, m);
-            rs3 += __shfl_xor(rs3, m);
-        }
-        if (l16 == 0) {
-            atomicAdd(&rsum[lrow + 0], rs0);
-            atomicAdd(&rsum[lrow + 1], rs1);
-            atomicAdd(&rsum[lrow + 2], rs2);
-            atomicAdd(&rsum[lrow + 3], rs3);
-        }
-    }
-    __syncthreads();
-    if (tid < 128) atomicAdd(&w[(long)b * Nn + i0 + tid], rsum[tid]);
-}
-
-__global__ __launch_bounds__(256) void head_kernel(
-    const float* __restrict__ vpart, const float* __restrict__ mpart,
-    const float* __restrict__ Wrel2, const float* __restrict__ Wroot2,
-    const float* __restrict__ brel2,
-    const float* __restrict__ W1, const float* __restrict__ b1,
-    const float* __restrict__ Wout, const float* __restrict__ bout,
-    float* __restrict__ out)
-{
-    int b = blockIdx.x;
-    int j = threadIdx.x;
-    __shared__ float vs[Hh], ms[Hh], gs[Hh], g2[Hh];
-    float vp = 0.f, mp = 0.f;
-    #pragma unroll
-    for (int p = 0; p < 8; ++p) {
-        long o = ((long)(b * 8 + p)) * Hh + j;
-        vp += vpart[o];
-        mp += mpart[o];
-    }
-    vs[j] = vp * (1.0f / (float)Nn);
-    ms[j] = mp * (1.0f / (float)Nn);
-    __syncthreads();
-    float s = brel2[j];
-    for (int c = 0; c < Hh; ++c)
-        s += vs[c] * Wrel2[c * Hh + j] + ms[c] * Wroot2[c * Hh + j];
-    gs[j] = s;
-    __syncthreads();
-    float t = b1[j];
-    for (int k = 0; k < Hh; ++k) t += gs[k] * W1[k * Hh + j];
-    g2[j] = fmaxf(t, 0.f);
-    __syncthreads();
-    if (j < OUTD) {
-        float s2 = bout[j];
-        for (int k = 0; k < Hh; ++k) s2 += g2[k] * Wout[k * OUTD + j];
-        out[b * OUTD + j] = s2;
+        if (act && j < OUTD) {
+            float s2 = bout[j];
+            for (int k = 0; k < Hh; ++k) s2 += g2[k] * Wout[k * OUTD + j];
+            out[blk * OUTD + j] = s2;
+        }
     }
 }
 
@@ -653,34 +641,16 @@
     const float* Wout   = (const float*)d_in[18];
     const float* bout   = (const float*)d_in[19];
     float* out = (float*)d_out;
-
     char* ws = (char*)d_ws;
-    unsigned short* h0b  = (unsigned short*)(ws + 16777216);
-    unsigned short* h0T  = (unsigned short*)(ws + 25165824);
-    float*          sq   = (float*)(ws + 33554432);
-    unsigned short* Aadj = (unsigned short*)(ws + 33685504);
-    unsigned short* h1b  = (unsigned short*)(ws + 84017152);
-    unsigned short* h1T  = (unsigned short*)(ws + 100794368);
-    unsigned short* WrelT0  = (unsigned short*)(ws + 167903232);
-    unsigned short* WrootT0 = (unsigned short*)(ws + 167968768);
-    unsigned short* WrelT1  = (unsigned short*)(ws + 168034304);
-    unsigned short* WrootT1 = (unsigned short*)(ws + 168165376);
-    float*          w     = (float*)(ws + 168558592);
-    float*          vpart = (float*)(ws + 168689664);
-    float*          mpart = (float*)(ws + 169213952);
-
-    prep_h0<<<1152, 256, 0, stream>>>(x, Wg, bg, Wrel0, Wroot0, Wrel1, Wroot1,
-                                      WrelT0, WrootT0, WrelT1, WrootT1,
-                                      w, h0b, h0T, sq);
-
-    gram_A_mfma<<<dim3(16 * Bsz, 1, 1), 512, 0, stream>>>(h0b, sq, sigma, Aadj, w);
-
-    fused_l0<<<dim3(4 * Bsz, 1, 1), 512, 0, stream>>>(
-        h0T, Aadj, h0b, WrelT0, WrootT0, brel0, h1b, h1T);
-
-    fused_l1<<<dim3(4 * Bsz, 1, 1), 512, 0, stream>>>(
-        h1T, Aadj, h1b, WrelT1, WrootT1, brel1, w, vpart, mpart);
-
-    head_kernel<<<Bsz, 256, 0, stream>>>(vpart, mpart, Wrel2, Wroot2, brel2,
-                                         W1, b1, Wout, bout, out);
+
+    void* kargs[] = {
+        (void*)&x, (void*)&sigma, (void*)&Wg, (void*)&bg,
+        (void*)&Wrel0, (void*)&Wroot0, (void*)&brel0,
+        (void*)&Wrel1, (void*)&Wroot1, (void*)&brel1,
+        (void*)&Wrel2, (void*)&Wroot2, (void*)&brel2,
+        (void*)&W1, (void*)&b1, (void*)&Wout, (void*)&bout,
+        (void*)&out, (void*)&ws
+    };
+    hipLaunchCooperativeKernel((const void*)mega, dim3(256), dim3(512),
+                               kargs, 0, stream);
 }
```

Result: slower. 676.1 us (+219.6%).
